# Kernel tuning notes

Hardware: AMD Instinct MI355X
Metric: run time of the kernel (lower is better)

Reference implementation:

```python
import jax, jax.numpy as jnp
import numpy as np

HIDDEN = 1024
HEADS = 16
HEAD_DIM = HIDDEN // HEADS
B, L = 2, 2048
EPS = 1e-5


def setup_inputs() -> dict:
    key = jax.random.key(0)
    ks = jax.random.split(key, 16)
    s = 0.02
    inp = {
        "hidden_state": jax.random.normal(ks[0], (B, L, HIDDEN), jnp.float32),
        "uncertainty_embedding": jax.random.normal(ks[1], (B, HIDDEN), jnp.float32),
        "attention_mask": jnp.ones((B, L), jnp.int32),
        # projection weights stored (in, out): y = x @ W + b
        "Wq": jax.random.normal(ks[2], (HIDDEN, HIDDEN), jnp.float32) * s,
        "bq": jnp.zeros((HIDDEN,), jnp.float32),
        "Wk": jax.random.normal(ks[3], (HIDDEN, HIDDEN), jnp.float32) * s,
        "bk": jnp.zeros((HIDDEN,), jnp.float32),
        "Wv": jax.random.normal(ks[4], (HIDDEN, HIDDEN), jnp.float32) * s,
        "bv": jnp.zeros((HIDDEN,), jnp.float32),
        "Wo": jax.random.normal(ks[5], (HIDDEN, HIDDEN), jnp.float32) * s,
        "bo": jnp.zeros((HIDDEN,), jnp.float32),
        # uncertainty_scale MLP: hidden -> hidden//4 -> num_heads
        "Wu1": jax.random.normal(ks[6], (HIDDEN, HIDDEN // 4), jnp.float32) * s,
        "bu1": jnp.zeros((HIDDEN // 4,), jnp.float32),
        "Wu2": jax.random.normal(ks[7], (HIDDEN // 4, HEADS), jnp.float32) * s,
        "bu2": jnp.zeros((HEADS,), jnp.float32),
        # LayerNorm
        "gamma": jnp.ones((HIDDEN,), jnp.float32),
        "beta": jnp.zeros((HIDDEN,), jnp.float32),
    }
    return inp


def _forward(hidden_state, uncertainty_embedding, attention_mask,
             Wq, bq, Wk, bk, Wv, bv, Wo, bo, Wu1, bu1, Wu2, bu2, gamma, beta):
    Bb, Ll, _ = hidden_state.shape
    # projections -> (B, H, L, Dh)
    def split_heads(x):
        return x.reshape(Bb, Ll, HEADS, HEAD_DIM).transpose(0, 2, 1, 3)
    Q = split_heads(hidden_state @ Wq + bq)
    K = split_heads(hidden_state @ Wk + bk)
    V = split_heads(hidden_state @ Wv + bv)

    scores = jnp.einsum('bhqd,bhkd->bhqk', Q, K) / (HEAD_DIM ** 0.5)
    mask = (attention_mask == 0)[:, None, None, :]  # (B,1,1,L) over key dim
    scores = jnp.where(mask, -1e9, scores)

    # per-head uncertainty gate in (0,1)
    u = jax.nn.relu(uncertainty_embedding @ Wu1 + bu1)
    scale = jax.nn.sigmoid(u @ Wu2 + bu2)  # (B, H)
    scores = scores * scale[:, :, None, None]

    attn = jax.nn.softmax(scores, axis=-1)
    out = jnp.einsum('bhqk,bhkd->bhqd', attn, V)
    out = out.transpose(0, 2, 1, 3).reshape(Bb, Ll, HIDDEN)
    out = out @ Wo + bo

    y = hidden_state + out
    mu = jnp.mean(y, axis=-1, keepdims=True)
    var = jnp.var(y, axis=-1, keepdims=True)
    return (y - mu) * jax.lax.rsqrt(var + EPS) * gamma + beta


def reference(hidden_state, uncertainty_embedding, attention_mask,
              Wq, bq, Wk, bk, Wv, bv, Wo, bo, Wu1, bu1, Wu2, bu2, gamma, beta):
    return _forward(hidden_state, uncertainty_embedding, attention_mask,
                    Wq, bq, Wk, bk, Wv, bv, Wo, bo, Wu1, bu1, Wu2, bu2, gamma, beta)
```

## Files before the change

### kernel.cpp

```cpp
#include <hip/hip_runtime.h>
#include <hip/hip_bf16.h>

#define HID 1024
#define NHEADS 16
#define DH 64
#define BB 2
#define LL 2048
#define MM (BB*LL)
#define EPSF 1e-5f

typedef __attribute__((ext_vector_type(8))) short bf16x8;
typedef __attribute__((ext_vector_type(4))) float f32x4;

#define MFMA16(A,Bf,C) __builtin_amdgcn_mfma_f32_16x16x32_bf16(A,Bf,C,0,0,0)
#define GLOAD_LDS16(G, Ld) \
  __builtin_amdgcn_global_load_lds((__attribute__((address_space(1))) const void*)(G), \
                                   (__attribute__((address_space(3))) void*)(Ld), 16, 0, 0)
#define PIN(v) asm("" : "+v"(v))
#define EXP2R(x) ({ float _y; asm("v_exp_f32 %0, %1" : "=v"(_y) : "v"(x)); _y; })

__device__ __forceinline__ unsigned short f2bf(float f) {
  union { float f; unsigned int u; } x; x.f = f;
  unsigned int r = x.u + 0x7fffu + ((x.u >> 16) & 1u);
  return (unsigned short)(r >> 16);
}

__global__ __launch_bounds__(256) void u1_partial(const float* __restrict__ ue,
                                                  const float* __restrict__ Wu1,
                                                  float* __restrict__ upart) {
  int b = blockIdx.y, kb = blockIdx.x;
  __shared__ float su[128];
  int tid = threadIdx.x;
  if (tid < 128) su[tid] = ue[b*HID + kb*128 + tid];
  __syncthreads();
  float s = 0.f;
  const float* w = Wu1 + (size_t)(kb*128)*256 + tid;
  for (int k = 0; k < 128; ++k) s += su[k] * w[(size_t)k*256];
  upart[(b*8 + kb)*256 + tid] = s;
}

__global__ __launch_bounds__(256) void u2_scale(const float* __restrict__ upart,
                                                const float* __restrict__ bu1,
                                                const float* __restrict__ Wu2,
                                                const float* __restrict__ bu2,
                                                float* __restrict__ scale) {
  int b = blockIdx.x, tid = threadIdx.x;
  __shared__ float su[256];
  float s = 0.f;
  for (int kb = 0; kb < 8; ++kb) s += upart[(b*8 + kb)*256 + tid];
  su[tid] = fmaxf(s + bu1[tid], 0.f);
  __syncthreads();
  if (tid < 16) {
    float a = bu2[tid];
    for (int k = 0; k < 256; ++k) a += su[k] * Wu2[k*16 + tid];
    scale[b*NHEADS + tid] = 1.f / (1.f + __expf(-a));
  }
}

__global__ __launch_bounds__(256) void maskprep_kernel(const int* __restrict__ amask,
                                                       const float* __restrict__ scale,
                                                       float* __restrict__ maskf) {
  int i = blockIdx.x*256 + threadIdx.x;
  int base = i*8;
  int bh = base >> 11;
  int b  = bh >> 4;
  float cm = scale[bh] * 1.44269504f;
  int k = base & (LL-1);
  #pragma unroll
  for (int j = 0; j < 8; ++j)
    maskf[base + j] = (amask[b*LL + k + j] == 0 ? -1e9f : 0.f) * cm - 16.f;
}

__global__ __launch_bounds__(256) void convert_x_kernel(const float* __restrict__ X,
                                                        unsigned short* __restrict__ Xb) {
  int i = blockIdx.x*256 + threadIdx.x;
  float4 v = ((const float4*)X)[i];
  ushort4 o; o.x = f2bf(v.x); o.y = f2bf(v.y); o.z = f2bf(v.z); o.w = f2bf(v.w);
  ((ushort4*)Xb)[i] = o;
}

__global__ void transw_kernel(const float* __restrict__ Wq, const float* __restrict__ Wk,
                              const float* __restrict__ Wv, const float* __restrict__ Wo,
                              unsigned short* __restrict__ Wqkvt, unsigned short* __restrict__ Wot) {
  __shared__ float tile[32][33];
  int z = blockIdx.z;
  const float* W = (z==0) ? Wq : (z==1) ? Wk : (z==2) ? Wv : Wo;
  unsigned short* dst = (z < 3) ? (Wqkvt + (size_t)z*HID*HID) : Wot;
  int n0 = blockIdx.x*32, k0 = blockIdx.y*32;
  int tx = threadIdx.x, ty = threadIdx.y;
  #pragma unroll
  for (int i = 0; i < 4; ++i) tile[ty+8*i][tx] = W[(size_t)(k0+ty+8*i)*HID + n0+tx];
  __syncthreads();
  #pragma unroll
  for (int i = 0; i < 4; ++i) dst[(size_t)(n0+ty+8*i)*HID + k0+tx] = f2bf(tile[tx][ty+8*i]);
}

template<int MODE>
__global__ __launch_bounds__(256) void gemm_kernel(
    const unsigned short* __restrict__ A,
    const unsigned short* __restrict__ Bt,
    const float* __restrict__ bias0, const float* __restrict__ bias1, const float* __restrict__ bias2,
    const float* __restrict__ resid,
    unsigned short* __restrict__ outQKV,
    float* __restrict__ outY) {
  constexpr int BM = (MODE == 0) ? 128 : 64;
  constexpr int MI = BM / 32;
  __shared__ alignas(16) unsigned short sA[BM*64];
  __shared__ alignas(16) unsigned short sB[128*64];
  const int tid = threadIdx.x, lane = tid & 63, wv = tid >> 6;
  const int wr = wv >> 1, wc = wv & 1;
  const int bid = blockIdx.x, xcd = bid & 7, loc = bid >> 3;
  const int nIdx = (MODE == 0) ? (xcd*3 + loc % 3) : xcd;
  const int mIdx = (MODE == 0) ? (loc / 3) : loc;
  const int m0 = mIdx*BM, n0 = nIdx*128;
  const int r = lane & 15, g = lane >> 4;

  const unsigned short* pA[MI];
  const unsigned short* pB[4];
  int ldsA[MI], ldsB[4];
  #pragma unroll
  for (int c = 0; c < MI; ++c) {
    const int base = c*4096 + wv*1024;
    const int po = base + lane*16;
    const int uo = po ^ (((po>>7)&7)<<4);
    const int e  = uo >> 1;
    pA[c] = A + (size_t)(m0 + (e>>6))*HID + (e&63);
    ldsA[c] = base;
  }
  #pragma unroll
  for (int c = 0; c < 4; ++c) {
    const int base = c*4096 + wv*1024;
    const int po = base + lane*16;
    const int uo = po ^ (((po>>7)&7)<<4);
    const int e  = uo >> 1;
    pB[c] = Bt + (size_t)(n0 + (e>>6))*HID + (e&63);
    ldsB[c] = base;
  }
  const int sw = (r & 7) << 4;
  int oALo = (wr*(MI*16) + r)*128 + ((g*16) ^ sw);
  int oAHi = (wr*(MI*16) + r)*128 + ((64 + g*16) ^ sw);
  int oBLo = (wc*64 + r)*128 + ((g*16) ^ sw);
  int oBHi = (wc*64 + r)*128 + ((64 + g*16) ^ sw);
  PIN(oALo); PIN(oAHi); PIN(oBLo); PIN(oBHi);

  f32x4 acc[MI][4];
  #pragma unroll
  for (int i = 0; i < MI; ++i)
    #pragma unroll
    for (int j = 0; j < 4; ++j) acc[i][j] = (f32x4){0.f,0.f,0.f,0.f};

  for (int k0 = 0; k0 < HID; k0 += 64) {
    #pragma unroll
    for (int c = 0; c < MI; ++c) {
      GLOAD_LDS16(pA[c], (char*)sA + ldsA[c]);
      pA[c] += 64;
    }
    #pragma unroll
    for (int c = 0; c < 4; ++c) {
      GLOAD_LDS16(pB[c], (char*)sB + ldsB[c]);
      pB[c] += 64;
    }
    __syncthreads();
    #pragma unroll
    for (int kk = 0; kk < 2; ++kk) {
      bf16x8 af[MI], bfv[4];
      #pragma unroll
      for (int i = 0; i < MI; ++i)
        af[i]  = *(const bf16x8*)((const char*)sA + (kk ? oAHi : oALo) + i*2048);
      #pragma unroll
      for (int j = 0; j < 4; ++j)
        bfv[j] = *(const bf16x8*)((const char*)sB + (kk ? oBHi : oBLo) + j*2048);
      __builtin_amdgcn_s_setprio(1);
      #pragma unroll
      for (int i = 0; i < MI; ++i)
        #pragma unroll
        for (int j = 0; j < 4; ++j)
          acc[i][j] = MFMA16(af[i], bfv[j], acc[i][j]);
      __builtin_amdgcn_s_setprio(0);
    }
    __syncthreads();
  }

  if (MODE == 0) {
    const int which = n0 >> 10;
    const float* bias = (which==0) ? bias0 : (which==1) ? bias1 : bias2;
    if (which < 2) {
      unsigned short* dst = outQKV + (size_t)which * ((size_t)MM*HID);
      #pragma unroll
      for (int i = 0; i < MI; ++i)
        #pragma unroll
        for (int j = 0; j < 4; ++j)
          #pragma unroll
          for (int rr = 0; rr < 4; ++rr) {
            int row = m0 + wr*(MI*16) + i*16 + g*4 + rr;
            int col = n0 + wc*64 + j*16 + r;
            int nn = col & (HID-1);
            int hh = nn >> 6, d = nn & 63;
            int bI = row >> 11, l = row & (LL-1);
            float v = acc[i][j][rr] + bias[nn];
            dst[(((size_t)(bI*NHEADS + hh)*LL + l) << 6) + d] = f2bf(v);
          }
    } else {
      unsigned short* dst = outQKV + 2*((size_t)MM*HID);
      #pragma unroll
      for (int i = 0; i < MI; ++i)
        #pragma unroll
        for (int j = 0; j < 4; ++j) {
          int col = n0 + wc*64 + j*16 + r;
          int nn = col & (HID-1);
          int hh = nn >> 6, d = nn & 63;
          int row0 = m0 + wr*(MI*16) + i*16 + g*4;
          int bI = row0 >> 11, l0 = row0 & (LL-1);
          ushort4 o4;
          o4.x = f2bf(acc[i][j][0] + bias[nn]);
          o4.y = f2bf(acc[i][j][1] + bias[nn]);
          o4.z = f2bf(acc[i][j][2] + bias[nn]);
          o4.w = f2bf(acc[i][j][3] + bias[nn]);
          *(ushort4*)(dst + ((size_t)((bI*NHEADS + hh)*DH + d))*LL + l0) = o4;
        }
    }
  } else {
    #pragma unroll
    for (int i = 0; i < MI; ++i)
      #pragma unroll
      for (int j = 0; j < 4; ++j)
        #pragma unroll
        for (int rr = 0; rr < 4; ++rr) {
          int row = m0 + wr*(MI*16) + i*16 + g*4 + rr;
          int col = n0 + wc*64 + j*16 + r;
          size_t idx = (size_t)row*HID + col;
          outY[idx] = acc[i][j][rr] + bias0[col] + resid[idx];
        }
  }
}

__global__ __launch_bounds__(256, 4) void attn_kernel(
    const unsigned short* __restrict__ Qb,
    const unsigned short* __restrict__ Kb,
    const unsigned short* __restrict__ Vt,
    const float* __restrict__ maskf,
    const float* __restrict__ scale_ws,
    unsigned short* __restrict__ attnout) {
  __shared__ alignas(16) unsigned short sK[64*64];
  __shared__ alignas(16) unsigned short sV[64*64];
  __shared__ alignas(16) unsigned short sP[4][16*64];
  const int p = blockIdx.x;
  const int bh = (p & 7)*4 + ((p >> 3) >> 5);
  const int q0 = ((p >> 3) & 31) * 64;
  const int b  = bh >> 4;
  const int tid = threadIdx.x, lane = tid & 63, wv = tid >> 6;
  const int r = lane & 15, g = lane >> 4;
  const size_t hoff = (size_t)bh * (LL*DH);
  const float c2 = 0.125f * scale_ws[bh] * 1.44269504f;

  int soff[2], srow[2], sco[2];
  #pragma unroll
  for (int ro = 0; ro < 2; ++ro) {
    srow[ro] = (tid + ro*256) >> 3;
    sco[ro]  = (tid & 7) * 8;
    soff[ro] = srow[ro]*128 + ((sco[ro]*2) ^ ((srow[ro]&7)<<4));
  }
  PIN(soff[0]); PIN(soff[1]);

  const unsigned short* pK0 = Kb + hoff + (size_t)srow[0]*DH + sco[0];
  const unsigned short* pK1 = Kb + hoff + (size_t)srow[1]*DH + sco[1];
  const unsigned short* pV0 = Vt + hoff + (size_t)srow[0]*LL + sco[0];
  const unsigned short* pV1 = Vt + hoff + (size_t)srow[1]*LL + sco[1];
  const float* pm = maskf + (size_t)bh*LL + g*4;

  const int sw = (r & 7) << 4;
  int oLo = r*128 + ((g*16) ^ sw);
  int oHi = r*128 + ((64 + g*16) ^ sw);
  PIN(oLo); PIN(oHi);
  int wP[4];
  #pragma unroll
  for (int kt = 0; kt < 4; ++kt) {
    wP[kt] = r*128 + ((kt*32 + g*8) ^ sw);
    PIN(wP[kt]);
  }

  bf16x8 aQ[2];
  {
    const int qrow = q0 + wv*16 + r;
    #pragma unroll
    for (int kc = 0; kc < 2; ++kc)
      aQ[kc] = *(const bf16x8*)(Qb + hoff + (size_t)qrow*DH + kc*32 + g*8);
  }
  const short ONE_BF = (short)0x3F80;
  const bf16x8 vone = {ONE_BF,ONE_BF,ONE_BF,ONE_BF,ONE_BF,ONE_BF,ONE_BF,ONE_BF};

  f32x4 accO[4];
  #pragma unroll
  for (int j = 0; j < 4; ++j) accO[j] = (f32x4){0.f,0.f,0.f,0.f};
  f32x4 lsum = (f32x4){0.f,0.f,0.f,0.f};

  bf16x8 kr0 = *(const bf16x8*)pK0;  pK0 += 64*DH;
  bf16x8 kr1 = *(const bf16x8*)pK1;  pK1 += 64*DH;
  bf16x8 vr0 = *(const bf16x8*)pV0;  pV0 += 64;
  bf16x8 vr1 = *(const bf16x8*)pV1;  pV1 += 64;
  float4 mreg[4];
  #pragma unroll
  for (int kt = 0; kt < 4; ++kt) mreg[kt] = *(const float4*)(pm + kt*16);
  pm += 64;

  for (int t = 0; t < LL/64; ++t) {
    __builtin_amdgcn_s_barrier();
    *(bf16x8*)((char*)sK + soff[0]) = kr0;
    *(bf16x8*)((char*)sK + soff[1]) = kr1;
    *(bf16x8*)((char*)sV + soff[0]) = vr0;
    *(bf16x8*)((char*)sV + soff[1]) = vr1;
    if (t + 1 < LL/64) {
      kr0 = *(const bf16x8*)pK0;  pK0 += 64*DH;
      kr1 = *(const bf16x8*)pK1;  pK1 += 64*DH;
      vr0 = *(const bf16x8*)pV0;  pV0 += 64;
      vr1 = *(const bf16x8*)pV1;  pV1 += 64;
    }
    asm volatile("s_waitcnt lgkmcnt(0)" ::: "memory");
    __builtin_amdgcn_s_barrier();
    __builtin_amdgcn_sched_barrier(0);

    f32x4 sc[4];
    __builtin_amdgcn_s_setprio(1);
    #pragma unroll
    for (int kt = 0; kt < 4; ++kt) {
      bf16x8 bk0 = *(const bf16x8*)((const char*)sK + oLo + kt*2048);
      bf16x8 bk1 = *(const bf16x8*)((const char*)sK + oHi + kt*2048);
      f32x4 a = (f32x4){0.f,0.f,0.f,0.f};
      a = MFMA16(bk0, aQ[0], a);
      a = MFMA16(bk1, aQ[1], a);
      sc[kt] = a;
    }
    __builtin_amdgcn_s_setprio(0);

    #pragma unroll
    for (int kt = 0; kt < 4; ++kt) {
      sc[kt][0] = EXP2R(sc[kt][0]*c2 + mreg[kt].x);
      sc[kt][1] = EXP2R(sc[kt][1]*c2 + mreg[kt].y);
      sc[kt][2] = EXP2R(sc[kt][2]*c2 + mreg[kt].z);
      sc[kt][3] = EXP2R(sc[kt][3]*c2 + mreg[kt].w);
    }
    if (t + 1 < LL/64) {
      #pragma unroll
      for (int kt = 0; kt < 4; ++kt) mreg[kt] = *(const float4*)(pm + kt*16);
      pm += 64;
    }

    char* sPw = (char*)sP[wv];
    #pragma unroll
    for (int kt = 0; kt < 4; ++kt) {
      unsigned int lo, hi;
      asm("v_cvt_pk_bf16_f32 %0, %1, %2" : "=v"(lo) : "v"(sc[kt][0]), "v"(sc[kt][1]));
      asm("v_cvt_pk_bf16_f32 %0, %1, %2" : "=v"(hi) : "v"(sc[kt][2]), "v"(sc[kt][3]));
      uint2 w; w.x = lo; w.y = hi;
      *(uint2*)(sPw + wP[kt]) = w;
    }
    bf16x8 aP0 = *(const bf16x8*)(sPw + oLo);
    bf16x8 aP1 = *(const bf16x8*)(sPw + oHi);

    lsum = MFMA16(vone, aP0, lsum);
    lsum = MFMA16(vone, aP1, lsum);

    __builtin_amdgcn_s_setprio(1);
    #pragma unroll
    for (int j = 0; j < 4; ++j) {
      bf16x8 v0 = *(const bf16x8*)((const char*)sV + oLo + j*2048);
      bf16x8 v1 = *(const bf16x8*)((const char*)sV + oHi + j*2048);
      accO[j] = MFMA16(v0, aP0, accO[j]);
      accO[j] = MFMA16(v1, aP1, accO[j]);
    }
    __builtin_amdgcn_s_setprio(0);
  }

  const float invl = 1.f / lsum[0];
  const int qq = q0 + wv*16 + r;
  #pragma unroll
  for (int j = 0; j < 4; ++j) {
    ushort4 o4;
    o4.x = f2bf(accO[j][0] * invl);
    o4.y = f2bf(accO[j][1] * invl);
    o4.z = f2bf(accO[j][2] * invl);
    o4.w = f2bf(accO[j][3] * invl);
    const int col = (bh & 15)*DH + j*16 + g*4;
    *(ushort4*)(attnout + (size_t)(b*LL + qq)*HID + col) = o4;
  }
}

__global__ __launch_bounds__(256) void ln_kernel(const float* __restrict__ Y,
                                                 const float* __restrict__ gamma,
                                                 const float* __restrict__ beta,
                                                 float* __restrict__ out) {
  int row = blockIdx.x, tid = threadIdx.x;
  const float* y = Y + (size_t)row*HID;
  float v[4]; float s = 0.f, s2 = 0.f;
  #pragma unroll
  for (int i = 0; i < 4; ++i) { v[i] = y[tid + i*256]; s += v[i]; s2 += v[i]*v[i]; }
  #pragma unroll
  for (int o = 1; o < 64; o <<= 1) { s += __shfl_xor(s, o, 64); s2 += __shfl_xor(s2, o, 64); }
  __shared__ float ws1[4], ws2[4];
  if ((tid & 63) == 0) { ws1[tid>>6] = s; ws2[tid>>6] = s2; }
  __syncthreads();
  s  = ws1[0] + ws1[1] + ws1[2] + ws1[3];
  s2 = ws2[0] + ws2[1] + ws2[2] + ws2[3];
  float mu  = s * (1.f/HID);
  float var = s2 * (1.f/HID) - mu*mu;
  float rs  = rsqrtf(var + EPSF);
  #pragma unroll
  for (int i = 0; i < 4; ++i) {
    int c = tid + i*256;
    out[(size_t)row*HID + c] = (v[i] - mu)*rs*gamma[c] + beta[c];
  }
}

extern "C" void kernel_launch(void* const* d_in, const int* in_sizes, int n_in,
                              void* d_out, int out_size, void* d_ws, size_t ws_size,
                              hipStream_t stream) {
  const float* hidden = (const float*)d_in[0];
  const float* ue     = (const float*)d_in[1];
  const int*   amask  = (const int*)d_in[2];
  const float* Wq = (const float*)d_in[3];  const float* bq = (const float*)d_in[4];
  const float* Wk = (const float*)d_in[5];  const float* bk = (const float*)d_in[6];
  const float* Wv = (const float*)d_in[7];  const float* bv = (const float*)d_in[8];
  const float* Wo = (const float*)d_in[9];  const float* bo = (const float*)d_in[10];
  const float* Wu1 = (const float*)d_in[11]; const float* bu1 = (const float*)d_in[12];
  const float* Wu2 = (const float*)d_in[13]; const float* bu2 = (const float*)d_in[14];
  const float* gamma = (const float*)d_in[15]; const float* beta = (const float*)d_in[16];
  float* out = (float*)d_out;

  char* ws = (char*)d_ws;
  if (ws_size < ((56u<<20) + 32768)) return;
  unsigned short* Xbf   = (unsigned short*)(ws + 0);
  float*          Y     = (float*)(ws + 0);
  float*          maskf = (float*)(ws + (8u<<20));
  unsigned short* Wqkvt = (unsigned short*)(ws + (16u<<20));
  unsigned short* Wot   = (unsigned short*)(ws + (22u<<20));
  unsigned short* Qb    = (unsigned short*)(ws + (24u<<20));
  unsigned short* Kb    = Qb + (size_t)MM*HID;
  unsigned short* Vb    = Kb + (size_t)MM*HID;
  unsigned short* AOut  = (unsigned short*)(ws + (48u<<20));
  float* upart = (float*)(ws + (56u<<20));
  float* scale = upart + BB*8*256;

  u1_partial<<<dim3(8, BB), 256, 0, stream>>>(ue, Wu1, upart);
  u2_scale<<<BB, 256, 0, stream>>>(upart, bu1, Wu2, bu2, scale);
  maskprep_kernel<<<(BB*NHEADS*LL/8)/256, 256, 0, stream>>>(amask, scale, maskf);
  convert_x_kernel<<<(MM*HID/4)/256, 256, 0, stream>>>(hidden, Xbf);
  transw_kernel<<<dim3(32, 32, 4), dim3(32, 8), 0, stream>>>(Wq, Wk, Wv, Wo, Wqkvt, Wot);
  gemm_kernel<0><<<768, 256, 0, stream>>>(Xbf, Wqkvt,
                                          bq, bk, bv, nullptr, Qb, nullptr);
  attn_kernel<<<BB*NHEADS*(LL/64), 256, 0, stream>>>(Qb, Kb, Vb, maskf, scale, AOut);
  gemm_kernel<1><<<512, 256, 0, stream>>>(AOut, Wot,
                                          bo, nullptr, nullptr, hidden, nullptr, Y);
  ln_kernel<<<MM, 256, 0, stream>>>(Y, gamma, beta, out);
}
```

Baseline: 149.1 us.

## Double-buffer LDS tiles with async global-to-LDS loads in GEMM and attention

The GEMM main loop now uses two LDS buffers, so the global_load_lds for the next K-tile is issued before the MFMAs on the current tile run. This replaces the earlier load-then-sync-then-compute pattern with its two barriers per step. The attention kernel drops the register-staged K/V copy into LDS and uses double-buffered direct global-to-LDS loads with the same swizzle. It waits with vmcnt(0) plus one barrier per tile. In exchange LDS use doubles, which may reduce occupancy, and the full vmcnt wait also waits on the mask prefetch loads.

```diff
diff --git a/kernel.cpp b/kernel.cpp
--- a/kernel.cpp
+++ b/kernel.cpp
@@ -18,6 +18,11 @@
                                    (__attribute__((address_space(3))) void*)(Ld), 16, 0, 0)
 #define PIN(v) asm("" : "+v"(v))
 #define EXP2R(x) ({ float _y; asm("v_exp_f32 %0, %1" : "=v"(_y) : "v"(x)); _y; })
+#define WAIT_VM0_BAR() do { \
+    asm volatile("s_waitcnt vmcnt(0)" ::: "memory"); \
+    __builtin_amdgcn_s_barrier(); \
+    __builtin_amdgcn_sched_barrier(0); \
+  } while (0)
 
 __device__ __forceinline__ unsigned short f2bf(float f) {
   union { float f; unsigned int u; } x; x.f = f;
@@ -105,8 +110,10 @@
     float* __restrict__ outY) {
   constexpr int BM = (MODE == 0) ? 128 : 64;
   constexpr int MI = BM / 32;
-  __shared__ alignas(16) unsigned short sA[BM*64];
-  __shared__ alignas(16) unsigned short sB[128*64];
+  constexpr int ASZ = BM*64*2;
+  constexpr int BSZ = 128*64*2;
+  __shared__ alignas(16) unsigned short sA[2*BM*64];
+  __shared__ alignas(16) unsigned short sB[2*128*64];
   const int tid = threadIdx.x, lane = tid & 63, wv = tid >> 6;
   const int wr = wv >> 1, wc = wv & 1;
   const int bid = blockIdx.x, xcd = bid & 7, loc = bid >> 3;
@@ -143,43 +150,56 @@
   int oBHi = (wc*64 + r)*128 + ((64 + g*16) ^ sw);
   PIN(oALo); PIN(oAHi); PIN(oBLo); PIN(oBHi);
 
+#define GSTAGE(BUF) do {                                                      \
+    _Pragma("unroll")                                                         \
+    for (int c = 0; c < MI; ++c) {                                            \
+      GLOAD_LDS16(pA[c], (char*)sA + (BUF)*ASZ + ldsA[c]); pA[c] += 64;       \
+    }                                                                         \
+    _Pragma("unroll")                                                         \
+    for (int c = 0; c < 4; ++c) {                                             \
+      GLOAD_LDS16(pB[c], (char*)sB + (BUF)*BSZ + ldsB[c]); pB[c] += 64;       \
+    }                                                                         \
+  } while (0)
+
+#define GCOMPUTE(BUF) do {                                                    \
+    _Pragma("unroll")                                                         \
+    for (int kk = 0; kk < 2; ++kk) {                                          \
+      bf16x8 af[MI], bfv[4];                                                  \
+      _Pragma("unroll")                                                       \
+      for (int i = 0; i < MI; ++i)                                            \
+        af[i]  = *(const bf16x8*)((const char*)sA + (BUF)*ASZ +               \
+                                  (kk ? oAHi : oALo) + i*2048);               \
+      _Pragma("unroll")                                                       \
+      for (int j = 0; j < 4; ++j)                                             \
+        bfv[j] = *(const bf16x8*)((const char*)sB + (BUF)*BSZ +               \
+                                  (kk ? oBHi : oBLo) + j*2048);               \
+      __builtin_amdgcn_s_setprio(1);                                          \
+      _Pragma("unroll")                                                       \
+      for (int i = 0; i < MI; ++i)                                            \
+        _Pragma("unroll")                                                     \
+        for (int j = 0; j < 4; ++j)                                           \
+          acc[i][j] = MFMA16(af[i], bfv[j], acc[i][j]);                       \
+      __builtin_amdgcn_s_setprio(0);                                          \
+    }                                                                         \
+  } while (0)
+
   f32x4 acc[MI][4];
   #pragma unroll
   for (int i = 0; i < MI; ++i)
     #pragma unroll
     for (int j = 0; j < 4; ++j) acc[i][j] = (f32x4){0.f,0.f,0.f,0.f};
 
-  for (int k0 = 0; k0 < HID; k0 += 64) {
-    #pragma unroll
-    for (int c = 0; c < MI; ++c) {
-      GLOAD_LDS16(pA[c], (char*)sA + ldsA[c]);
-      pA[c] += 64;
-    }
-    #pragma unroll
-    for (int c = 0; c < 4; ++c) {
-      GLOAD_LDS16(pB[c], (char*)sB + ldsB[c]);
-      pB[c] += 64;
-    }
-    __syncthreads();
-    #pragma unroll
-    for (int kk = 0; kk < 2; ++kk) {
-      bf16x8 af[MI], bfv[4];
-      #pragma unroll
-      for (int i = 0; i < MI; ++i)
-        af[i]  = *(const bf16x8*)((const char*)sA + (kk ? oAHi : oALo) + i*2048);
-      #pragma unroll
-      for (int j = 0; j < 4; ++j)
-        bfv[j] = *(const bf16x8*)((const char*)sB + (kk ? oBHi : oBLo) + j*2048);
-      __builtin_amdgcn_s_setprio(1);
-      #pragma unroll
-      for (int i = 0; i < MI; ++i)
-        #pragma unroll
-        for (int j = 0; j < 4; ++j)
-          acc[i][j] = MFMA16(af[i], bfv[j], acc[i][j]);
-      __builtin_amdgcn_s_setprio(0);
-    }
-    __syncthreads();
-  }
+  GSTAGE(0);
+  for (int k0 = 0; k0 < HID; k0 += 128) {
+    WAIT_VM0_BAR();
+    GSTAGE(1);
+    GCOMPUTE(0);
+    WAIT_VM0_BAR();
+    if (k0 + 128 < HID) GSTAGE(0);
+    GCOMPUTE(1);
+  }
+#undef GSTAGE
+#undef GCOMPUTE
 
   if (MODE == 0) {
     const int which = n0 >> 10;
@@ -241,8 +261,8 @@
     const float* __restrict__ maskf,
     const float* __restrict__ scale_ws,
     unsigned short* __restrict__ attnout) {
-  __shared__ alignas(16) unsigned short sK[64*64];
-  __shared__ alignas(16) unsigned short sV[64*64];
+  __shared__ alignas(16) unsigned short sK[2*64*64];
+  __shared__ alignas(16) unsigned short sV[2*64*64];
   __shared__ alignas(16) unsigned short sP[4][16*64];
   const int p = blockIdx.x;
   const int bh = (p & 7)*4 + ((p >> 3) >> 5);
@@ -252,21 +272,23 @@
   const int r = lane & 15, g = lane >> 4;
   const size_t hoff = (size_t)bh * (LL*DH);
   const float c2 = 0.125f * scale_ws[bh] * 1.44269504f;
-
-  int soff[2], srow[2], sco[2];
-  #pragma unroll
-  for (int ro = 0; ro < 2; ++ro) {
-    srow[ro] = (tid + ro*256) >> 3;
-    sco[ro]  = (tid & 7) * 8;
-    soff[ro] = srow[ro]*128 + ((sco[ro]*2) ^ ((srow[ro]&7)<<4));
-  }
-  PIN(soff[0]); PIN(soff[1]);
-
-  const unsigned short* pK0 = Kb + hoff + (size_t)srow[0]*DH + sco[0];
-  const unsigned short* pK1 = Kb + hoff + (size_t)srow[1]*DH + sco[1];
-  const unsigned short* pV0 = Vt + hoff + (size_t)srow[0]*LL + sco[0];
-  const unsigned short* pV1 = Vt + hoff + (size_t)srow[1]*LL + sco[1];
+  const unsigned short* Kg = Kb + hoff;
+  const unsigned short* Vg = Vt + hoff;
   const float* pm = maskf + (size_t)bh*LL + g*4;
+
+  const unsigned short* pKs[2];
+  const unsigned short* pVs[2];
+  int lbase[2];
+  #pragma unroll
+  for (int c = 0; c < 2; ++c) {
+    const int base_ = c*4096 + wv*1024;
+    const int po_ = base_ + lane*16;
+    const int uo_ = po_ ^ (((po_>>7)&7)<<4);
+    const int e_  = uo_ >> 1;
+    pKs[c] = Kg + (size_t)(e_>>6)*DH + (e_&63);
+    pVs[c] = Vg + (size_t)(e_>>6)*LL + (e_&63);
+    lbase[c] = base_;
+  }
 
   const int sw = (r & 7) << 4;
   int oLo = r*128 + ((g*16) ^ sw);
@@ -294,82 +316,80 @@
   for (int j = 0; j < 4; ++j) accO[j] = (f32x4){0.f,0.f,0.f,0.f};
   f32x4 lsum = (f32x4){0.f,0.f,0.f,0.f};
 
-  bf16x8 kr0 = *(const bf16x8*)pK0;  pK0 += 64*DH;
-  bf16x8 kr1 = *(const bf16x8*)pK1;  pK1 += 64*DH;
-  bf16x8 vr0 = *(const bf16x8*)pV0;  pV0 += 64;
-  bf16x8 vr1 = *(const bf16x8*)pV1;  pV1 += 64;
+  #pragma unroll
+  for (int c = 0; c < 2; ++c) {
+    GLOAD_LDS16(pKs[c], (char*)sK + lbase[c]);
+    GLOAD_LDS16(pVs[c], (char*)sV + lbase[c]);
+    pKs[c] += 64*DH;  pVs[c] += 64;
+  }
   float4 mreg[4];
   #pragma unroll
   for (int kt = 0; kt < 4; ++kt) mreg[kt] = *(const float4*)(pm + kt*16);
   pm += 64;
 
-  for (int t = 0; t < LL/64; ++t) {
-    __builtin_amdgcn_s_barrier();
-    *(bf16x8*)((char*)sK + soff[0]) = kr0;
-    *(bf16x8*)((char*)sK + soff[1]) = kr1;
-    *(bf16x8*)((char*)sV + soff[0]) = vr0;
-    *(bf16x8*)((char*)sV + soff[1]) = vr1;
-    if (t + 1 < LL/64) {
-      kr0 = *(const bf16x8*)pK0;  pK0 += 64*DH;
-      kr1 = *(const bf16x8*)pK1;  pK1 += 64*DH;
-      vr0 = *(const bf16x8*)pV0;  pV0 += 64;
-      vr1 = *(const bf16x8*)pV1;  pV1 += 64;
-    }
-    asm volatile("s_waitcnt lgkmcnt(0)" ::: "memory");
-    __builtin_amdgcn_s_barrier();
-    __builtin_amdgcn_sched_barrier(0);
-
-    f32x4 sc[4];
-    __builtin_amdgcn_s_setprio(1);
-    #pragma unroll
-    for (int kt = 0; kt < 4; ++kt) {
-      bf16x8 bk0 = *(const bf16x8*)((const char*)sK + oLo + kt*2048);
-      bf16x8 bk1 = *(const bf16x8*)((const char*)sK + oHi + kt*2048);
-      f32x4 a = (f32x4){0.f,0.f,0.f,0.f};
-      a = MFMA16(bk0, aQ[0], a);
-      a = MFMA16(bk1, aQ[1], a);
-      sc[kt] = a;
-    }
-    __builtin_amdgcn_s_setprio(0);
-
-    #pragma unroll
-    for (int kt = 0; kt < 4; ++kt) {
-      sc[kt][0] = EXP2R(sc[kt][0]*c2 + mreg[kt].x);
-      sc[kt][1] = EXP2R(sc[kt][1]*c2 + mreg[kt].y);
-      sc[kt][2] = EXP2R(sc[kt][2]*c2 + mreg[kt].z);
-      sc[kt][3] = EXP2R(sc[kt][3]*c2 + mreg[kt].w);
-    }
-    if (t + 1 < LL/64) {
-      #pragma unroll
-      for (int kt = 0; kt < 4; ++kt) mreg[kt] = *(const float4*)(pm + kt*16);
-      pm += 64;
-    }
-
-    char* sPw = (char*)sP[wv];
-    #pragma unroll
-    for (int kt = 0; kt < 4; ++kt) {
-      unsigned int lo, hi;
-      asm("v_cvt_pk_bf16_f32 %0, %1, %2" : "=v"(lo) : "v"(sc[kt][0]), "v"(sc[kt][1]));
-      asm("v_cvt_pk_bf16_f32 %0, %1, %2" : "=v"(hi) : "v"(sc[kt][2]), "v"(sc[kt][3]));
-      uint2 w; w.x = lo; w.y = hi;
-      *(uint2*)(sPw + wP[kt]) = w;
-    }
-    bf16x8 aP0 = *(const bf16x8*)(sPw + oLo);
-    bf16x8 aP1 = *(const bf16x8*)(sPw + oHi);
-
-    lsum = MFMA16(vone, aP0, lsum);
-    lsum = MFMA16(vone, aP1, lsum);
-
-    __builtin_amdgcn_s_setprio(1);
-    #pragma unroll
-    for (int j = 0; j < 4; ++j) {
-      bf16x8 v0 = *(const bf16x8*)((const char*)sV + oLo + j*2048);
-      bf16x8 v1 = *(const bf16x8*)((const char*)sV + oHi + j*2048);
-      accO[j] = MFMA16(v0, aP0, accO[j]);
-      accO[j] = MFMA16(v1, aP1, accO[j]);
-    }
-    __builtin_amdgcn_s_setprio(0);
-  }
+#define ATILE(CUROFF, NBOFF, T) do {                                          \
+    WAIT_VM0_BAR();                            \
+    if ((T) + 1 < LL/64) {                     \
+      _Pragma("unroll")                                                       \
+      for (int c = 0; c < 2; ++c) {                                           \
+        GLOAD_LDS16(pKs[c], (char*)sK + (NBOFF) + lbase[c]);                  \
+        GLOAD_LDS16(pVs[c], (char*)sV + (NBOFF) + lbase[c]);                  \
+        pKs[c] += 64*DH;  pVs[c] += 64;                                       \
+      }                                                                       \
+    }                                                                         \
+    f32x4 sc[4];                                                              \
+    __builtin_amdgcn_s_setprio(1);                                            \
+    _Pragma("unroll")                                                         \
+    for (int kt = 0; kt < 4; ++kt) {                                          \
+      bf16x8 bk0 = *(const bf16x8*)((const char*)sK + (CUROFF) + oLo + kt*2048); \
+      bf16x8 bk1 = *(const bf16x8*)((const char*)sK + (CUROFF) + oHi + kt*2048); \
+      f32x4 a = (f32x4){0.f,0.f,0.f,0.f};                                     \
+      a = MFMA16(bk0, aQ[0], a);                                              \
+      a = MFMA16(bk1, aQ[1], a);                                              \
+      sc[kt] = a;                                                             \
+    }                                                                         \
+    __builtin_amdgcn_s_setprio(0);                                            \
+    _Pragma("unroll")                                                         \
+    for (int kt = 0; kt < 4; ++kt) {                                          \
+      sc[kt][0] = EXP2R(sc[kt][0]*c2 + mreg[kt].x);                           \
+      sc[kt][1] = EXP2R(sc[kt][1]*c2 + mreg[kt].y);                           \
+      sc[kt][2] = EXP2R(sc[kt][2]*c2 + mreg[kt].z);                           \
+      sc[kt][3] = EXP2R(sc[kt][3]*c2 + mreg[kt].w);                           \
+    }                                                                         \
+    if ((T) + 1 < LL/64) {                                                    \
+      _Pragma("unroll")                                                       \
+      for (int kt = 0; kt < 4; ++kt) mreg[kt] = *(const float4*)(pm + kt*16); \
+      pm += 64;                                                               \
+    }                                                                         \
+    char* sPw = (char*)sP[wv];                                                \
+    _Pragma("unroll")                                                         \
+    for (int kt = 0; kt < 4; ++kt) {                                          \
+      unsigned int lo, hi;                                                    \
+      asm("v_cvt_pk_bf16_f32 %0, %1, %2" : "=v"(lo) : "v"(sc[kt][0]), "v"(sc[kt][1])); \
+      asm("v_cvt_pk_bf16_f32 %0, %1, %2" : "=v"(hi) : "v"(sc[kt][2]), "v"(sc[kt][3])); \
+      uint2 w; w.x = lo; w.y = hi;                                            \
+      *(uint2*)(sPw + wP[kt]) = w;                                            \
+    }                                                                         \
+    bf16x8 aP0 = *(const bf16x8*)(sPw + oLo);                                 \
+    bf16x8 aP1 = *(const bf16x8*)(sPw + oHi);                                 \
+    lsum = MFMA16(vone, aP0, lsum);                                           \
+    lsum = MFMA16(vone, aP1, lsum);                                           \
+    __builtin_amdgcn_s_setprio(1);                                            \
+    _Pragma("unroll")                                                         \
+    for (int j = 0; j < 4; ++j) {                                             \
+      bf16x8 v0 = *(const bf16x8*)((const char*)sV + (CUROFF) + oLo + j*2048); \
+      bf16x8 v1 = *(const bf16x8*)((const char*)sV + (CUROFF) + oHi + j*2048); \
+      accO[j] = MFMA16(v0, aP0, accO[j]);                                     \
+      accO[j] = MFMA16(v1, aP1, accO[j]);                                     \
+    }                                                                         \
+    __builtin_amdgcn_s_setprio(0);                                            \
+  } while (0)
+
+  for (int t = 0; t < LL/64; t += 2) {
+    ATILE(0,    8192, t);
+    ATILE(8192, 0,    t+1);
+  }
+#undef ATILE
 
   const float invl = 1.f / lsum[0];
   const int qq = q0 + wv*16 + r;
```

Measured after the change: 144.8 us. 2.9% less time.
